# Kernel optimization log

Measured on AMD Instinct MI355X. Metric: run time of the kernel, lower is better.

The kernel has to match this reference:

```python
import jax, jax.numpy as jnp
import numpy as np

# FlowNetC correlation config (matches init_kwargs)
PAD = 20           # pad_size
MAX_DISP = 20      # max_displacement
STRIDE2 = 2        # displacement stride
K = 1              # kernel_size (1x1 patch)
# stride1 = 1, corr_multiply = 1 (multiply mode)

GRID_RAD = MAX_DISP // STRIDE2           # 10
N_DISP = (2 * GRID_RAD + 1) ** 2         # 441 output channels


def _disp_offsets():
    # slice start offsets into the padded input2 for each displacement
    # (dy, dx) in {-GRID_RAD..GRID_RAD} * STRIDE2; start = PAD + d (pad == max_disp)
    d = np.arange(-GRID_RAD, GRID_RAD + 1) * STRIDE2
    dy, dx = np.meshgrid(d, d, indexing='ij')  # row-major: dy outer, dx inner
    return np.stack([PAD + dy.ravel(), PAD + dx.ravel()], axis=1).astype(np.int32)  # [441,2]


def setup_inputs() -> dict:
    key = jax.random.key(0)
    k1, k2 = jax.random.split(key)
    B, C, H, W = 8, 256, 64, 64
    input1 = jax.random.normal(k1, (B, C, H, W), dtype=jnp.float32)
    input2 = jax.random.normal(k2, (B, C, H, W), dtype=jnp.float32)
    return {"input1": input1, "input2": input2}


def reference(input1, input2):
    B, C, H, W = input1.shape
    sumelems = float(K * K * C)  # normalization used by the CUDA kernel
    # zero-pad input2 spatially by PAD (pad_size == max_displacement)
    x2p = jnp.pad(input2, ((0, 0), (0, 0), (PAD, PAD), (PAD, PAD)))
    offs = jnp.asarray(_disp_offsets())  # [441, 2] int32

    def step(carry, off):
        # window of input2 displaced by (dy, dx) relative to input1
        sl = jax.lax.dynamic_slice(x2p, (0, 0, off[0], off[1]), (B, C, H, W))
        corr = jnp.sum(input1 * sl, axis=1) / sumelems  # [B, H, W]
        return carry, corr

    _, out = jax.lax.scan(step, None, offs)       # [441, B, H, W]
    return jnp.transpose(out, (1, 0, 2, 3))       # [B, 441, H, W]
```

## Files before the change

kernel.cpp:

```cpp
#include <hip/hip_runtime.h>
#include <hip/hip_bf16.h>


typedef short    bf16x8 __attribute__((ext_vector_type(8)));
typedef float    f32x4  __attribute__((ext_vector_type(4)));

constexpr int CSTRIDE = 64 * 64;
constexpr int BSTRIDE = 256 * CSTRIDE;

union BF2 { __hip_bfloat162 h; unsigned u; };
union BF1 { __hip_bfloat16 h; unsigned short u; };

__device__ inline unsigned pack_bf2(float lo, float hi) {
    BF2 cv;
    cv.h = __float22bfloat162_rn(make_float2(lo, hi));
    return cv.u;
}

__device__ __align__(16) const uint4 ZERO16 = {0u, 0u, 0u, 0u};

__global__ __launch_bounds__(256)
void conv_in2(const float* __restrict__ in2, unsigned* __restrict__ out_dw)
{
    __shared__ unsigned short lt[64 * 66];
    const int tid = threadIdx.x;
    const int b = blockIdx.x & 7;
    const int y = blockIdx.x >> 3;
    const float* src = in2 + b * BSTRIDE + y * 64;
    unsigned* odw = out_dw + (b * 64 + y) * 8192;

    for (int c0 = 0; c0 < 256; c0 += 64) {
        __syncthreads();
#pragma unroll
        for (int it = 0; it < 16; ++it) {
            const int c = it * 4 + (tid >> 6);
            const int x = tid & 63;
            BF1 cv; cv.h = __float2bfloat16(src[(c0 + c) * CSTRIDE + x]);
            lt[x * 66 + c] = cv.u;
        }
        __syncthreads();
        const unsigned* ldw = reinterpret_cast<const unsigned*>(lt);
#pragma unroll
        for (int it = 0; it < 8; ++it) {
            const int d   = tid + 256 * it;
            const int c8g = d >> 8;
            const int x   = (d >> 2) & 63;
            const int cd2 = d & 3;
            odw[((c0 >> 3) + c8g) * 256 + x * 4 + cd2] = ldw[x * 33 + c8g * 4 + cd2];
        }
    }
}

__global__ __launch_bounds__(1024, 4)
void corr_mfma(const float* __restrict__ in1,
               const uint4* __restrict__ in2t,
               float* __restrict__ out)
{
    __shared__ float slds[2][2][21 * 65];

    const int tid  = threadIdx.x;
    const int lane = tid & 63;
    const int w    = tid >> 6;
    const int cl   = lane & 15;
    const int q    = lane >> 4;
    const int m    = w & 3;
    const int n    = m + (w >> 2);
    const int b    = blockIdx.x & 7;
    const int p    = blockIdx.x >> 3;
    const int y0   = 4 * (p >> 1) + (p & 1);

    bf16x8 af[2][8];
#pragma unroll
    for (int h = 0; h < 2; ++h) {
        const float* pb = in1 + b * BSTRIDE + (y0 + 2 * h) * 64 + 16 * m + cl
                        + 8 * q * CSTRIDE;
#pragma unroll
        for (int k = 0; k < 8; ++k) {
            const float* pp = pb + 32 * k * CSTRIDE;
            float v[8];
#pragma unroll
            for (int j = 0; j < 8; ++j) v[j] = pp[j * CSTRIDE];
#pragma unroll
            for (int j = 0; j < 4; ++j)
                ((unsigned*)&af[h][k])[j] = pack_bf2(v[2 * j], v[2 * j + 1]);
        }
    }

    const int  x    = 16 * n + cl - 20;
    const bool xok  = (x >= 0) && (x < 64);
    const int  gcol = 16 * n + cl;

    for (int i = 0; i < 22; ++i) {
        const int  yy      = y0 - 20 + 2 * i;
        const bool compute = (yy >= 0) && (yy < 64);
        const int  ib      = i & 1;

        if (compute) {
            const uint4* src = in2t + (b * 64 + yy) * 2048 + x;
            f32x4 acc0 = {0.f, 0.f, 0.f, 0.f};
            f32x4 acc1 = {0.f, 0.f, 0.f, 0.f};
#pragma unroll
            for (int k = 0; k < 8; ++k) {
                const uint4* pk = xok ? (src + (4 * k + q) * 64) : &ZERO16;
                const uint4  wv = *pk;
                const bf16x8 bf = __builtin_bit_cast(bf16x8, wv);
                acc0 = __builtin_amdgcn_mfma_f32_16x16x32_bf16(af[0][k], bf, acc0, 0, 0, 0);
                acc1 = __builtin_amdgcn_mfma_f32_16x16x32_bf16(af[1][k], bf, acc1, 0, 0, 0);
            }
#pragma unroll
            for (int i4 = 0; i4 < 4; ++i4) {
                const int gx = 16 * m + 4 * q + i4;
                const int d2 = gcol - gx;
                if (d2 >= 0 && d2 <= 40 && !(d2 & 1)) {
                    slds[ib][0][(d2 >> 1) * 65 + gx] = acc0[i4];
                    slds[ib][1][(d2 >> 1) * 65 + gx] = acc1[i4];
                }
            }
        }
        __syncthreads();

        const int r0 = i, r1 = i - 1;
#pragma unroll
        for (int t3 = 0; t3 < 3; ++t3) {
            const int t = tid + 1024 * t3;
            if (t < 2 * 21 * 64) {
                const int h  = (t >= 1344) ? 1 : 0;
                const int u  = t - 1344 * h;
                const int dx = u >> 6, gx = u & 63;
                const int r  = h ? r1 : r0;
                if (r >= 0 && r <= 20) {
                    const float val = compute ? slds[ib][h][dx * 65 + gx] * (1.f / 256.f)
                                              : 0.f;
                    out[((b * 441 + r * 21 + dx) * 64 + y0 + 2 * h) * 64 + gx] = val;
                }
            }
        }
    }
}

extern "C" void kernel_launch(void* const* d_in, const int* in_sizes, int n_in,
                              void* d_out, int out_size, void* d_ws, size_t ws_size,
                              hipStream_t stream) {
    const float* in1 = (const float*)d_in[0];
    const float* in2 = (const float*)d_in[1];
    float* out = (float*)d_out;

    conv_in2<<<dim3(512), dim3(256), 0, stream>>>(in2, (unsigned*)d_ws);
    corr_mfma<<<dim3(256), dim3(1024), 0, stream>>>(in1, (const uint4*)d_ws, out);
}
```

Before: 150.3 us.

## Double-buffer input2 rows in LDS via async global_load_lds and simplify conversion kernel

The correlation kernel now stages each 64KB bf16 row of input2 into LDS with global_load_lds direct-to-LDS loads, prefetching the next row while computing the current one, instead of each wave reading global memory directly per MFMA. The conversion kernel drops the LDS transpose and packs eight channels per thread directly into 16-byte stores. The aim is to hide global load latency and cut redundant global reads. In exchange, LDS use grows by 64KB per block, which may limit occupancy, and the explicit waitcnt plus barrier adds synchronisation.

```diff
diff --git a/kernel.cpp b/kernel.cpp
--- a/kernel.cpp
+++ b/kernel.cpp
@@ -9,7 +9,6 @@
 constexpr int BSTRIDE = 256 * CSTRIDE;
 
 union BF2 { __hip_bfloat162 h; unsigned u; };
-union BF1 { __hip_bfloat16 h; unsigned short u; };
 
 __device__ inline unsigned pack_bf2(float lo, float hi) {
     BF2 cv;
@@ -17,38 +16,37 @@
     return cv.u;
 }
 
-__device__ __align__(16) const uint4 ZERO16 = {0u, 0u, 0u, 0u};
-
 __global__ __launch_bounds__(256)
-void conv_in2(const float* __restrict__ in2, unsigned* __restrict__ out_dw)
+void conv_in2(const float* __restrict__ in2, uint4* __restrict__ out16)
 {
-    __shared__ unsigned short lt[64 * 66];
     const int tid = threadIdx.x;
     const int b = blockIdx.x & 7;
     const int y = blockIdx.x >> 3;
     const float* src = in2 + b * BSTRIDE + y * 64;
-    unsigned* odw = out_dw + (b * 64 + y) * 8192;
+    uint4* dst = out16 + (b * 64 + y) * 2048;
+#pragma unroll
+    for (int it = 0; it < 8; ++it) {
+        const int t  = tid + 256 * it;
+        const int c8 = t >> 6;
+        const int x  = t & 63;
+        const float* p = src + c8 * 8 * CSTRIDE + x;
+        float v[8];
+#pragma unroll
+        for (int j = 0; j < 8; ++j) v[j] = p[j * CSTRIDE];
+        uint4 o;
+        o.x = pack_bf2(v[0], v[1]);
+        o.y = pack_bf2(v[2], v[3]);
+        o.z = pack_bf2(v[4], v[5]);
+        o.w = pack_bf2(v[6], v[7]);
+        dst[c8 * 64 + x] = o;
+    }
+}
 
-    for (int c0 = 0; c0 < 256; c0 += 64) {
-        __syncthreads();
-#pragma unroll
-        for (int it = 0; it < 16; ++it) {
-            const int c = it * 4 + (tid >> 6);
-            const int x = tid & 63;
-            BF1 cv; cv.h = __float2bfloat16(src[(c0 + c) * CSTRIDE + x]);
-            lt[x * 66 + c] = cv.u;
-        }
-        __syncthreads();
-        const unsigned* ldw = reinterpret_cast<const unsigned*>(lt);
-#pragma unroll
-        for (int it = 0; it < 8; ++it) {
-            const int d   = tid + 256 * it;
-            const int c8g = d >> 8;
-            const int x   = (d >> 2) & 63;
-            const int cd2 = d & 3;
-            odw[((c0 >> 3) + c8g) * 256 + x * 4 + cd2] = ldw[x * 33 + c8g * 4 + cd2];
-        }
-    }
+__device__ inline void stage64(const uint4* __restrict__ gsrc, uint4* lds_dst) {
+    __builtin_amdgcn_global_load_lds(
+        (const __attribute__((address_space(1))) void*)gsrc,
+        (__attribute__((address_space(3))) void*)lds_dst,
+        16, 0, 0);
 }
 
 __global__ __launch_bounds__(1024, 4)
@@ -56,7 +54,9 @@
                const uint4* __restrict__ in2t,
                float* __restrict__ out)
 {
+    __shared__ __align__(16) uint4 rowbuf[2][2048];
     __shared__ float slds[2][2][21 * 65];
+    __shared__ __align__(16) uint4 zchunk;
 
     const int tid  = threadIdx.x;
     const int lane = tid & 63;
@@ -68,6 +68,8 @@
     const int b    = blockIdx.x & 7;
     const int p    = blockIdx.x >> 3;
     const int y0   = 4 * (p >> 1) + (p & 1);
+
+    if (tid == 0) { uint4 z = {0u, 0u, 0u, 0u}; zchunk = z; }
 
     bf16x8 af[2][8];
 #pragma unroll
@@ -90,20 +92,43 @@
     const bool xok  = (x >= 0) && (x < 64);
     const int  gcol = 16 * n + cl;
 
+    {
+        const int yy0 = y0 - 20;
+        if (yy0 >= 0) {
+            const uint4* rp = in2t + (b * 64 + yy0) * 2048;
+            const int c0 = w * 128 + lane;
+            stage64(rp + c0,      &rowbuf[0][w * 128]);
+            stage64(rp + c0 + 64, &rowbuf[0][w * 128 + 64]);
+        }
+    }
+    __builtin_amdgcn_sched_barrier(0);
+    asm volatile("s_waitcnt vmcnt(0) lgkmcnt(0)" ::: "memory");
+    __builtin_amdgcn_s_barrier();
+    __builtin_amdgcn_sched_barrier(0);
+
     for (int i = 0; i < 22; ++i) {
+        const int  ib      = i & 1;
         const int  yy      = y0 - 20 + 2 * i;
         const bool compute = (yy >= 0) && (yy < 64);
-        const int  ib      = i & 1;
+
+        {
+            const int yn = y0 - 20 + 2 * (i + 1);
+            if ((i + 1) < 22 && yn >= 0 && yn < 64) {
+                const uint4* rp = in2t + (b * 64 + yn) * 2048;
+                const int c0 = w * 128 + lane;
+                stage64(rp + c0,      &rowbuf[ib ^ 1][w * 128]);
+                stage64(rp + c0 + 64, &rowbuf[ib ^ 1][w * 128 + 64]);
+            }
+        }
 
         if (compute) {
-            const uint4* src = in2t + (b * 64 + yy) * 2048 + x;
             f32x4 acc0 = {0.f, 0.f, 0.f, 0.f};
             f32x4 acc1 = {0.f, 0.f, 0.f, 0.f};
+            const uint4* rbase = &rowbuf[ib][q * 64 + x];
 #pragma unroll
             for (int k = 0; k < 8; ++k) {
-                const uint4* pk = xok ? (src + (4 * k + q) * 64) : &ZERO16;
-                const uint4  wv = *pk;
-                const bf16x8 bf = __builtin_bit_cast(bf16x8, wv);
+                const uint4* pk = xok ? (rbase + k * 256) : &zchunk;
+                const bf16x8 bf = __builtin_bit_cast(bf16x8, *pk);
                 acc0 = __builtin_amdgcn_mfma_f32_16x16x32_bf16(af[0][k], bf, acc0, 0, 0, 0);
                 acc1 = __builtin_amdgcn_mfma_f32_16x16x32_bf16(af[1][k], bf, acc1, 0, 0, 0);
             }
@@ -117,7 +142,11 @@
                 }
             }
         }
-        __syncthreads();
+
+        __builtin_amdgcn_sched_barrier(0);
+        asm volatile("s_waitcnt vmcnt(0) lgkmcnt(0)" ::: "memory");
+        __builtin_amdgcn_s_barrier();
+        __builtin_amdgcn_sched_barrier(0);
 
         const int r0 = i, r1 = i - 1;
 #pragma unroll
@@ -145,6 +174,6 @@
     const float* in2 = (const float*)d_in[1];
     float* out = (float*)d_out;
 
-    conv_in2<<<dim3(512), dim3(256), 0, stream>>>(in2, (unsigned*)d_ws);
+    conv_in2<<<dim3(512), dim3(256), 0, stream>>>(in2, (uint4*)d_ws);
     corr_mfma<<<dim3(256), dim3(1024), 0, stream>>>(in1, (const uint4*)d_ws, out);
 }
```

After: 161.3 us. +7.3%, slower.

## Prefetch next row's B operand into registers and vectorize the in2 conversion

Applied to the files above, without the earlier changes.

The correlation kernel now loads the next displaced row of the bf16 input2 into registers while the current row's MFMAs and stores run, instead of loading from global memory right before each use. The full-block barrier becomes a raw s_barrier with an LDS-only waitcnt, and it runs only on iterations that actually compute. The conversion kernel drops its LDS transpose: it reads float4s across 8 channels and packs them straight into 16-byte bf16x8 stores. This costs more registers for the prefetch buffer and relies on the compute predicate being uniform across the block.

```diff
diff --git a/kernel.cpp b/kernel.cpp
--- a/kernel.cpp
+++ b/kernel.cpp
@@ -9,7 +9,6 @@
 constexpr int BSTRIDE = 256 * CSTRIDE;
 
 union BF2 { __hip_bfloat162 h; unsigned u; };
-union BF1 { __hip_bfloat16 h; unsigned short u; };
 
 __device__ inline unsigned pack_bf2(float lo, float hi) {
     BF2 cv;
@@ -17,37 +16,31 @@
     return cv.u;
 }
 
-__device__ __align__(16) const uint4 ZERO16 = {0u, 0u, 0u, 0u};
+#define ELT(v4, xi) ((xi) == 0 ? (v4).x : (xi) == 1 ? (v4).y : (xi) == 2 ? (v4).z : (v4).w)
 
-__global__ __launch_bounds__(256)
-void conv_in2(const float* __restrict__ in2, unsigned* __restrict__ out_dw)
+__global__ __launch_bounds__(512)
+void conv_in2(const float* __restrict__ in2, uint4* __restrict__ out16)
 {
-    __shared__ unsigned short lt[64 * 66];
     const int tid = threadIdx.x;
     const int b = blockIdx.x & 7;
     const int y = blockIdx.x >> 3;
-    const float* src = in2 + b * BSTRIDE + y * 64;
-    unsigned* odw = out_dw + (b * 64 + y) * 8192;
+    const int c8 = tid >> 4;
+    const int x0 = (tid & 15) * 4;
+    const float* p = in2 + b * BSTRIDE + y * 64 + c8 * 8 * CSTRIDE + x0;
+    uint4* dst = out16 + (b * 64 + y) * 2048 + c8 * 64 + x0;
 
-    for (int c0 = 0; c0 < 256; c0 += 64) {
-        __syncthreads();
+    float4 v[8];
 #pragma unroll
-        for (int it = 0; it < 16; ++it) {
-            const int c = it * 4 + (tid >> 6);
-            const int x = tid & 63;
-            BF1 cv; cv.h = __float2bfloat16(src[(c0 + c) * CSTRIDE + x]);
-            lt[x * 66 + c] = cv.u;
-        }
-        __syncthreads();
-        const unsigned* ldw = reinterpret_cast<const unsigned*>(lt);
+    for (int j = 0; j < 8; ++j)
+        v[j] = *reinterpret_cast<const float4*>(p + j * CSTRIDE);
 #pragma unroll
-        for (int it = 0; it < 8; ++it) {
-            const int d   = tid + 256 * it;
-            const int c8g = d >> 8;
-            const int x   = (d >> 2) & 63;
-            const int cd2 = d & 3;
-            odw[((c0 >> 3) + c8g) * 256 + x * 4 + cd2] = ldw[x * 33 + c8g * 4 + cd2];
-        }
+    for (int xi = 0; xi < 4; ++xi) {
+        uint4 o;
+        o.x = pack_bf2(ELT(v[0], xi), ELT(v[1], xi));
+        o.y = pack_bf2(ELT(v[2], xi), ELT(v[3], xi));
+        o.z = pack_bf2(ELT(v[4], xi), ELT(v[5], xi));
+        o.w = pack_bf2(ELT(v[6], xi), ELT(v[7], xi));
+        dst[xi] = o;
     }
 }
 
@@ -90,23 +83,45 @@
     const bool xok  = (x >= 0) && (x < 64);
     const int  gcol = 16 * n + cl;
 
+    uint4 breg[8];
+#pragma unroll
+    for (int k = 0; k < 8; ++k) breg[k] = uint4{0u, 0u, 0u, 0u};
+
+    {
+        const int yy0 = y0 - 20;
+        if (yy0 >= 0 && xok) {
+            const uint4* src = in2t + (b * 64 + yy0) * 2048 + q * 64 + x;
+#pragma unroll
+            for (int k = 0; k < 8; ++k) breg[k] = src[k * 256];
+        }
+    }
+
     for (int i = 0; i < 22; ++i) {
+        const int  ib      = i & 1;
         const int  yy      = y0 - 20 + 2 * i;
         const bool compute = (yy >= 0) && (yy < 64);
-        const int  ib      = i & 1;
 
+        f32x4 acc0 = {0.f, 0.f, 0.f, 0.f};
+        f32x4 acc1 = {0.f, 0.f, 0.f, 0.f};
         if (compute) {
-            const uint4* src = in2t + (b * 64 + yy) * 2048 + x;
-            f32x4 acc0 = {0.f, 0.f, 0.f, 0.f};
-            f32x4 acc1 = {0.f, 0.f, 0.f, 0.f};
 #pragma unroll
             for (int k = 0; k < 8; ++k) {
-                const uint4* pk = xok ? (src + (4 * k + q) * 64) : &ZERO16;
-                const uint4  wv = *pk;
-                const bf16x8 bf = __builtin_bit_cast(bf16x8, wv);
+                const bf16x8 bf = __builtin_bit_cast(bf16x8, breg[k]);
                 acc0 = __builtin_amdgcn_mfma_f32_16x16x32_bf16(af[0][k], bf, acc0, 0, 0, 0);
                 acc1 = __builtin_amdgcn_mfma_f32_16x16x32_bf16(af[1][k], bf, acc1, 0, 0, 0);
             }
+        }
+
+        {
+            const int yn = yy + 2;
+            if ((i + 1) < 22 && yn >= 0 && yn < 64 && xok) {
+                const uint4* src = in2t + (b * 64 + yn) * 2048 + q * 64 + x;
+#pragma unroll
+                for (int k = 0; k < 8; ++k) breg[k] = src[k * 256];
+            }
+        }
+
+        if (compute) {
 #pragma unroll
             for (int i4 = 0; i4 < 4; ++i4) {
                 const int gx = 16 * m + 4 * q + i4;
@@ -116,8 +131,11 @@
                     slds[ib][1][(d2 >> 1) * 65 + gx] = acc1[i4];
                 }
             }
+            __builtin_amdgcn_sched_barrier(0);
+            asm volatile("s_waitcnt lgkmcnt(0)" ::: "memory");
+            __builtin_amdgcn_s_barrier();
+            __builtin_amdgcn_sched_barrier(0);
         }
-        __syncthreads();
 
         const int r0 = i, r1 = i - 1;
 #pragma unroll
@@ -145,6 +163,6 @@
     const float* in2 = (const float*)d_in[1];
     float* out = (float*)d_out;
 
-    conv_in2<<<dim3(512), dim3(256), 0, stream>>>(in2, (unsigned*)d_ws);
+    conv_in2<<<dim3(512), dim3(512), 0, stream>>>(in2, (uint4*)d_ws);
     corr_mfma<<<dim3(256), dim3(1024), 0, stream>>>(in1, (const uint4*)d_ws, out);
 }
```

After: 181.1 us. +20.5%, slower.
